# Performance work log

Measured on AMD Instinct MI355X. Metric: run time of the kernel, lower is better.

Reference implementation:

```python
import jax, jax.numpy as jnp
import numpy as np

N_NODES = 100000
N_EDGES = 640000
D = 128
N_LAYERS = 4
N_GRAPHS = 512


def setup_inputs() -> dict:
    key = jax.random.key(0)
    ks = jax.random.split(key, 12)
    x = jax.random.normal(ks[0], (N_NODES, D), dtype=jnp.float32)
    edge_index = jax.random.randint(ks[1], (2, N_EDGES), 0, N_NODES, dtype=jnp.int64)
    batch = jnp.sort(jax.random.randint(ks[2], (N_NODES,), 0, N_GRAPHS, dtype=jnp.int64))
    s = 1.0 / np.sqrt(D)
    convW = jax.random.uniform(ks[3], (N_LAYERS, D, D), jnp.float32, -s, s)
    convB = jax.random.uniform(ks[4], (N_LAYERS, D), jnp.float32, -s, s)
    W1 = jax.random.uniform(ks[5], (D, D), jnp.float32, -s, s)
    b1 = jax.random.uniform(ks[6], (D,), jnp.float32, -s, s)
    W2 = jax.random.uniform(ks[7], (D, D), jnp.float32, -s, s)
    b2 = jax.random.uniform(ks[8], (D,), jnp.float32, -s, s)
    W3 = jax.random.uniform(ks[9], (D, 1), jnp.float32, -s, s)
    b3 = jax.random.uniform(ks[10], (1,), jnp.float32, -s, s)
    return {"x": x, "edge_index": edge_index, "batch": batch,
            "convW": convW, "convB": convB,
            "W1": W1, "b1": b1, "W2": W2, "b2": b2, "W3": W3, "b3": b3}


def reference(x, edge_index, batch, convW, convB, W1, b1, W2, b2, W3, b3):
    N = x.shape[0]
    # GCNConv default: add self-loops, symmetric deg^-1/2 normalization
    loops = jnp.arange(N, dtype=edge_index.dtype)
    src = jnp.concatenate([edge_index[0], loops])  # [E+N]
    dst = jnp.concatenate([edge_index[1], loops])
    deg = jax.ops.segment_sum(jnp.ones_like(dst, dtype=x.dtype), dst, num_segments=N)
    dinv = jnp.where(deg > 0, jax.lax.rsqrt(deg), 0.0)
    norm = (dinv[src] * dinv[dst])[:, None]  # [E+N, 1]
    h = x
    for i in range(N_LAYERS):
        hw = h @ convW[i]                                   # [N, D]
        msg = hw[src] * norm                                # gather + scale [E+N, D]
        agg = jax.ops.segment_sum(msg, dst, num_segments=N)  # scatter-add [N, D]
        h = jax.nn.relu(agg + convB[i])
    pooled = jax.ops.segment_sum(h, batch, num_segments=N_GRAPHS)  # [G, D]
    z = jax.nn.relu(pooled @ W1 + b1)
    z = jax.nn.relu(z @ W2 + b2)
    return jax.nn.sigmoid(z @ W3 + b3)  # [G, 1]
```

## Files before the change

### kernel.cpp

```cpp
#include <hip/hip_runtime.h>
#include <math.h>

#define D 128
#define LSTRIDE 136
#define NPB 64

typedef _Float16 half8 __attribute__((ext_vector_type(8)));
typedef _Float16 half4v __attribute__((ext_vector_type(4)));
typedef _Float16 half2v __attribute__((ext_vector_type(2)));
typedef float f32x4 __attribute__((ext_vector_type(4)));


__global__ void k_count(const int* __restrict__ ei, int* __restrict__ counts,
                        int* __restrict__ pidx, int E) {
    int e0 = (blockIdx.x * blockDim.x + threadIdx.x) * 4;
    if (e0 + 3 < E) {
        int4 d4 = *(const int4*)(ei + E + e0);
        int4 p;
        p.x = atomicAdd(&counts[d4.x], 1);
        p.y = atomicAdd(&counts[d4.y], 1);
        p.z = atomicAdd(&counts[d4.z], 1);
        p.w = atomicAdd(&counts[d4.w], 1);
        *(int4*)(pidx + e0) = p;
    } else {
        for (int e = e0; e < E; e++) pidx[e] = atomicAdd(&counts[ei[E + e]], 1);
    }
}

__global__ __launch_bounds__(256) void k_scan1(const int* __restrict__ counts,
                                               int* __restrict__ rowptr,
                                               int* __restrict__ bsums,
                                               float* __restrict__ dinv, int N) {
    __shared__ int sh[256];
    const int t = threadIdx.x;
    const int base = blockIdx.x * 1024 + t * 4;
    int c[4];
#pragma unroll
    for (int j = 0; j < 4; j++) c[j] = (base + j < N) ? counts[base + j] : 0;
#pragma unroll
    for (int j = 0; j < 4; j++)
        if (base + j < N) dinv[base + j] = rsqrtf((float)(c[j] + 1));
    int tsum = c[0] + c[1] + c[2] + c[3];
    sh[t] = tsum;
    __syncthreads();
    for (int off = 1; off < 256; off <<= 1) {
        int v = (t >= off) ? sh[t - off] : 0;
        __syncthreads();
        sh[t] += v;
        __syncthreads();
    }
    int run = (t == 0) ? 0 : sh[t - 1];
    if (t == 255) bsums[blockIdx.x] = sh[255];
#pragma unroll
    for (int j = 0; j < 4; j++) {
        if (base + j <= N) rowptr[base + j] = run;
        run += c[j];
    }
}

__global__ __launch_bounds__(128) void k_scan2(int* __restrict__ bsums, int NB) {
    __shared__ int sh[128];
    const int t = threadIdx.x;
    sh[t] = (t < NB) ? bsums[t] : 0;
    __syncthreads();
    for (int off = 1; off < 128; off <<= 1) {
        int v = (t >= off) ? sh[t - off] : 0;
        __syncthreads();
        sh[t] += v;
        __syncthreads();
    }
    if (t < NB) bsums[t] = (t == 0) ? 0 : sh[t - 1];
}

__global__ void k_scan3(int* __restrict__ rowptr, const int* __restrict__ bsums, int N) {
    int i = blockIdx.x * blockDim.x + threadIdx.x;
    if (i <= N) rowptr[i] += bsums[i >> 10];
}

__global__ void k_fill(const int* __restrict__ ei, const int* __restrict__ rowptr,
                       const int* __restrict__ pidx, int* __restrict__ srcs, int E) {
    int e0 = (blockIdx.x * blockDim.x + threadIdx.x) * 4;
    if (e0 + 3 < E) {
        int4 s4 = *(const int4*)(ei + e0);
        int4 d4 = *(const int4*)(ei + E + e0);
        int4 p4 = *(const int4*)(pidx + e0);
        int r0 = rowptr[d4.x], r1 = rowptr[d4.y], r2 = rowptr[d4.z], r3 = rowptr[d4.w];
        srcs[r0 + p4.x] = s4.x;
        srcs[r1 + p4.y] = s4.y;
        srcs[r2 + p4.z] = s4.z;
        srcs[r3 + p4.w] = s4.w;
    } else {
        for (int e = e0; e < E; e++)
            srcs[rowptr[ei[E + e]] + pidx[e]] = ei[e];
    }
}


__global__ void k_cvt(const float* __restrict__ x, const float* __restrict__ dinv,
                      _Float16* __restrict__ y, int n8) {
    int i = blockIdx.x * blockDim.x + threadIdx.x;
    if (i >= n8) return;
    float s = dinv[i >> 4];
    const float4 v0 = *(const float4*)(x + (size_t)i * 8);
    const float4 v1 = *(const float4*)(x + (size_t)i * 8 + 4);
    half8 h;
    h[0] = (_Float16)(v0.x * s); h[1] = (_Float16)(v0.y * s);
    h[2] = (_Float16)(v0.z * s); h[3] = (_Float16)(v0.w * s);
    h[4] = (_Float16)(v1.x * s); h[5] = (_Float16)(v1.y * s);
    h[6] = (_Float16)(v1.z * s); h[7] = (_Float16)(v1.w * s);
    *(half8*)(y + (size_t)i * 8) = h;
}


__global__ __launch_bounds__(256) void k_prepw(const float* __restrict__ convW,
                                               _Float16* __restrict__ Wf) {
    const int l = blockIdx.x >> 3;
    const int slot = (blockIdx.x & 7) * 256 + threadIdx.x;
    const float* W = convW + (size_t)l * D * D;
    const int p = slot >> 6, ln = slot & 63;
    const int s = p >> 3, c = p & 7;
    const int kbase = s * 32 + ((ln >> 4) << 3);
    const int n = (c << 4) + (ln & 15);
    half8 hv;
#pragma unroll
    for (int j = 0; j < 8; j++) hv[j] = (_Float16)W[(size_t)(kbase + j) * D + n];
    *(half8*)(Wf + (size_t)l * D * D + (size_t)slot * 8) = hv;
}


__global__ __launch_bounds__(256) void k_layer(
        const _Float16* __restrict__ gin,
        const int* __restrict__ rowptr, const int* __restrict__ srcs,
        const float* __restrict__ dinv,
        const _Float16* __restrict__ Wf,
        const float* __restrict__ bias,
        _Float16* __restrict__ gout, int N, int last) {
    __shared__ _Float16 S[NPB * LSTRIDE];

    const int tid  = threadIdx.x;
    const int w    = tid >> 6;
    const int lane = tid & 63;
    const int q    = lane >> 4;
    const int l16  = lane & 15;
    const int nb0  = blockIdx.x * NPB;

    const int cb = l16 * 8;
    for (int it = 0; it < 4; ++it) {
        const int nl = w * 16 + q * 4 + it;
        const int node = nb0 + nl;
        float a[8];
#pragma unroll
        for (int j = 0; j < 8; j++) a[j] = 0.f;

        if (node < N) {
            half8 sv = *(const half8*)(gin + (size_t)node * D + cb);
#pragma unroll
            for (int j = 0; j < 8; j++) a[j] = (float)sv[j];
            const int beg = rowptr[node];
            const int end = rowptr[node + 1];
            int e = beg;
            for (; e + 3 < end; e += 4) {
                int s0 = srcs[e], s1 = srcs[e + 1], s2 = srcs[e + 2], s3 = srcs[e + 3];
                half8 v0 = *(const half8*)(gin + (size_t)s0 * D + cb);
                half8 v1 = *(const half8*)(gin + (size_t)s1 * D + cb);
                half8 v2 = *(const half8*)(gin + (size_t)s2 * D + cb);
                half8 v3 = *(const half8*)(gin + (size_t)s3 * D + cb);
#pragma unroll
                for (int j = 0; j < 8; j++)
                    a[j] += ((float)v0[j] + (float)v1[j]) + ((float)v2[j] + (float)v3[j]);
            }
            for (; e < end; e++) {
                int s0 = srcs[e];
                half8 v0 = *(const half8*)(gin + (size_t)s0 * D + cb);
#pragma unroll
                for (int j = 0; j < 8; j++) a[j] += (float)v0[j];
            }
        }
        const float sc = (node < N) ? dinv[node] : 0.f;
        half8 o;
#pragma unroll
        for (int j = 0; j < 8; j++) o[j] = (_Float16)(a[j] * sc);
        *(half8*)(&S[nl * LSTRIDE + cb]) = o;
    }
    __syncthreads();

    f32x4 acc[8];
#pragma unroll
    for (int cc = 0; cc < 8; cc++) acc[cc] = (f32x4){0.f, 0.f, 0.f, 0.f};

    const int nl = w * 16 + l16;
#pragma unroll
    for (int s = 0; s < 4; s++) {
        half8 bf = *(const half8*)(&S[nl * LSTRIDE + s * 32 + q * 8]);
#pragma unroll
        for (int cc = 0; cc < 8; cc++) {
            half8 wh = *(const half8*)(Wf + (size_t)((s * 8 + cc) * 64 + lane) * 8);
            acc[cc] = __builtin_amdgcn_mfma_f32_16x16x32_f16(wh, bf, acc[cc], 0, 0, 0);
        }
    }

    const int node = nb0 + nl;
    if (node < N) {
        const float scale = last ? 1.0f : dinv[node];
        _Float16* rp = gout + (size_t)node * D + q * 4;
#pragma unroll
        for (int cc = 0; cc < 8; cc++) {
            const float4 bc = *(const float4*)(bias + cc * 16 + q * 4);
            half4v o;
            o[0] = (_Float16)(fmaxf(acc[cc][0] + bc.x, 0.f) * scale);
            o[1] = (_Float16)(fmaxf(acc[cc][1] + bc.y, 0.f) * scale);
            o[2] = (_Float16)(fmaxf(acc[cc][2] + bc.z, 0.f) * scale);
            o[3] = (_Float16)(fmaxf(acc[cc][3] + bc.w, 0.f) * scale);
            *(half4v*)(rp + cc * 16) = o;
        }
    }
}


__global__ __launch_bounds__(256) void k_poolhead(
        const _Float16* __restrict__ h, const int* __restrict__ batch,
        const float* __restrict__ W1, const float* __restrict__ b1,
        const float* __restrict__ W2, const float* __restrict__ b2,
        const float* __restrict__ W3, const float* __restrict__ b3,
        float* __restrict__ out, int N) {
    __shared__ int sb[2];
    __shared__ float part[4][D];
    __shared__ float v[D];
    __shared__ float z[D];
    __shared__ float red[D];

    const int g = blockIdx.x;
    const int t = threadIdx.x;

    if (t < 2) {
        int target = g + t;
        int lo = 0, hi = N;
        while (lo < hi) {
            int mid = (lo + hi) >> 1;
            if (batch[mid] < target) lo = mid + 1; else hi = mid;
        }
        sb[t] = lo;
    }
    __syncthreads();
    const int rs = sb[0], re = sb[1];

    const int w = t >> 6;
    const int lane = t & 63;
    const int c = lane * 2;

    float ax = 0.f, ay = 0.f;
    for (int r = rs + w; r < re; r += 4) {
        half2v vv = *(const half2v*)(h + (size_t)r * D + c);
        ax += (float)vv[0]; ay += (float)vv[1];
    }
    part[w][c] = ax;
    part[w][c + 1] = ay;
    __syncthreads();

    if (t < D) v[t] = part[0][t] + part[1][t] + part[2][t] + part[3][t];
    __syncthreads();

    if (t < D) {
        float s = b1[t];
        for (int k = 0; k < D; k++) s = fmaf(v[k], W1[(size_t)k * D + t], s);
        z[t] = fmaxf(s, 0.f);
    }
    __syncthreads();

    if (t < D) {
        float s = b2[t];
        for (int k = 0; k < D; k++) s = fmaf(z[k], W2[(size_t)k * D + t], s);
        red[t] = fmaxf(s, 0.f) * W3[t];
    }
    __syncthreads();
    for (int off = 64; off >= 1; off >>= 1) {
        if (t < off) red[t] += red[t + off];
        __syncthreads();
    }
    if (t == 0) out[g] = 1.f / (1.f + expf(-(red[0] + b3[0])));
}


extern "C" void kernel_launch(void* const* d_in, const int* in_sizes, int n_in,
                              void* d_out, int out_size, void* d_ws, size_t ws_size,
                              hipStream_t stream) {
    const float* x     = (const float*)d_in[0];
    const int*   ei    = (const int*)d_in[1];
    const int*   batch = (const int*)d_in[2];
    const float* convW = (const float*)d_in[3];
    const float* convB = (const float*)d_in[4];
    const float* W1 = (const float*)d_in[5];
    const float* b1 = (const float*)d_in[6];
    const float* W2 = (const float*)d_in[7];
    const float* b2 = (const float*)d_in[8];
    const float* W3 = (const float*)d_in[9];
    const float* b3 = (const float*)d_in[10];
    float* out = (float*)d_out;

    const int N = in_sizes[0] / D;
    const int E = in_sizes[1] / 2;
    const int G = out_size;
    const int NB = (N + 1023) / 1024;

    char* w = (char*)d_ws;
    size_t off = 0;
    auto alloc = [&](size_t bytes) -> char* {
        char* p = w + off;
        off += (bytes + 255) & ~(size_t)255;
        return p;
    };
    float*     dinv   = (float*)alloc((size_t)N * 4);
    _Float16*  gA     = (_Float16*)alloc((size_t)N * D * 2);
    _Float16*  gB     = (_Float16*)alloc((size_t)N * D * 2);
    _Float16*  Wf     = (_Float16*)alloc((size_t)4 * D * D * 2);
    int*       counts = (int*)alloc((size_t)N * 4);
    int*       rowptr = (int*)alloc((size_t)(N + 1) * 4);
    int*       pidx   = (int*)alloc((size_t)E * 4);
    int*       srcs   = (int*)alloc((size_t)E * 4);
    int*       bsums  = (int*)alloc((size_t)NB * 4);

    hipMemsetAsync(counts, 0, (size_t)N * 4, stream);
    k_count<<<(E / 4 + 255) / 256, 256, 0, stream>>>(ei, counts, pidx, E);
    k_prepw<<<32, 256, 0, stream>>>(convW, Wf);
    k_scan1<<<NB, 256, 0, stream>>>(counts, rowptr, bsums, dinv, N);
    k_cvt<<<(N * D / 8 + 255) / 256, 256, 0, stream>>>(x, dinv, gA, N * D / 8);
    k_scan2<<<1, 128, 0, stream>>>(bsums, NB);
    k_scan3<<<(N + 1 + 255) / 256, 256, 0, stream>>>(rowptr, bsums, N);
    k_fill<<<(E / 4 + 255) / 256, 256, 0, stream>>>(ei, rowptr, pidx, srcs, E);

    const int layer_grid = (N + NPB - 1) / NPB;
    const _Float16* gi = gA;
    _Float16* go = gB;
    for (int l = 0; l < 4; l++) {
        k_layer<<<layer_grid, 256, 0, stream>>>(gi, rowptr, srcs, dinv,
                                                Wf + (size_t)l * D * D,
                                                convB + (size_t)l * D,
                                                go, N, l == 3);
        const _Float16* tmp = go;
        go = (_Float16*)gi;
        gi = tmp;
    }

    k_poolhead<<<G, 256, 0, stream>>>(gi, batch, W1, b1, W2, b2, W3, b3, out, N);
}
```

Baseline: 388.7 us.

## Gather straight into MFMA operand registers and fuse block-sum scan into fixup

The layer kernel now has each wave own 16 nodes and each lane gather the 32 feature columns of one node that it later feeds to MFMA as the B operand. This removes the LDS staging buffer and the block-wide barrier. Within a wave, nodes are processed in lockstep two edges per step until the longest neighbour list in the wave is done, so lanes with short lists sit idle. Each row is read by only four lanes, so memory access is less coalesced than before. Separately, the single-block scan of block sums is folded into the rowptr fixup kernel: each block redoes the small prefix scan, which saves one kernel launch.

```diff
diff --git a/kernel.cpp b/kernel.cpp
--- a/kernel.cpp
+++ b/kernel.cpp
@@ -2,8 +2,6 @@
 #include <math.h>
 
 #define D 128
-#define LSTRIDE 136
-#define NPB 64
 
 typedef _Float16 half8 __attribute__((ext_vector_type(8)));
 typedef _Float16 half4v __attribute__((ext_vector_type(4)));
@@ -58,23 +56,24 @@
     }
 }
 
-__global__ __launch_bounds__(128) void k_scan2(int* __restrict__ bsums, int NB) {
-    __shared__ int sh[128];
+__global__ __launch_bounds__(256) void k_scan3(int* __restrict__ rowptr,
+                                               const int* __restrict__ bsums,
+                                               int NB, int N) {
+    __shared__ int pre[128];
     const int t = threadIdx.x;
-    sh[t] = (t < NB) ? bsums[t] : 0;
+    if (t < 128) pre[t] = (t < NB) ? bsums[t] : 0;
     __syncthreads();
     for (int off = 1; off < 128; off <<= 1) {
-        int v = (t >= off) ? sh[t - off] : 0;
-        __syncthreads();
-        sh[t] += v;
-        __syncthreads();
-    }
-    if (t < NB) bsums[t] = (t == 0) ? 0 : sh[t - 1];
-}
-
-__global__ void k_scan3(int* __restrict__ rowptr, const int* __restrict__ bsums, int N) {
-    int i = blockIdx.x * blockDim.x + threadIdx.x;
-    if (i <= N) rowptr[i] += bsums[i >> 10];
+        int v = (t >= off && t < 128) ? pre[t - off] : 0;
+        __syncthreads();
+        if (t < 128) pre[t] += v;
+        __syncthreads();
+    }
+    int i = blockIdx.x * blockDim.x + t;
+    if (i <= N) {
+        int b = i >> 10;
+        rowptr[i] += (b == 0) ? 0 : pre[b - 1];
+    }
 }
 
 __global__ void k_fill(const int* __restrict__ ei, const int* __restrict__ rowptr,
@@ -135,71 +134,85 @@
         const _Float16* __restrict__ Wf,
         const float* __restrict__ bias,
         _Float16* __restrict__ gout, int N, int last) {
-    __shared__ _Float16 S[NPB * LSTRIDE];
-
-    const int tid  = threadIdx.x;
-    const int w    = tid >> 6;
-    const int lane = tid & 63;
+    const int gtid = blockIdx.x * 256 + threadIdx.x;
+    const int wid  = gtid >> 6;
+    const int lane = threadIdx.x & 63;
     const int q    = lane >> 4;
     const int l16  = lane & 15;
-    const int nb0  = blockIdx.x * NPB;
-
-    const int cb = l16 * 8;
-    for (int it = 0; it < 4; ++it) {
-        const int nl = w * 16 + q * 4 + it;
-        const int node = nb0 + nl;
-        float a[8];
-#pragma unroll
-        for (int j = 0; j < 8; j++) a[j] = 0.f;
-
-        if (node < N) {
-            half8 sv = *(const half8*)(gin + (size_t)node * D + cb);
-#pragma unroll
-            for (int j = 0; j < 8; j++) a[j] = (float)sv[j];
-            const int beg = rowptr[node];
-            const int end = rowptr[node + 1];
-            int e = beg;
-            for (; e + 3 < end; e += 4) {
-                int s0 = srcs[e], s1 = srcs[e + 1], s2 = srcs[e + 2], s3 = srcs[e + 3];
-                half8 v0 = *(const half8*)(gin + (size_t)s0 * D + cb);
-                half8 v1 = *(const half8*)(gin + (size_t)s1 * D + cb);
-                half8 v2 = *(const half8*)(gin + (size_t)s2 * D + cb);
-                half8 v3 = *(const half8*)(gin + (size_t)s3 * D + cb);
-#pragma unroll
-                for (int j = 0; j < 8; j++)
-                    a[j] += ((float)v0[j] + (float)v1[j]) + ((float)v2[j] + (float)v3[j]);
+    const int node = wid * 16 + l16;
+    const int nodec = (node < N) ? node : (N - 1);
+
+    float af[4][8];
+    {
+        const _Float16* grow = gin + (size_t)nodec * D + q * 8;
+#pragma unroll
+        for (int s = 0; s < 4; s++) {
+            half8 v = *(const half8*)(grow + s * 32);
+#pragma unroll
+            for (int j = 0; j < 8; j++) af[s][j] = (float)v[j];
+        }
+    }
+
+    int e = rowptr[nodec];
+    const int end = rowptr[nodec + 1];
+    while (__any(e < end)) {
+        const int rem = end - e;
+        if (rem >= 2) {
+            int s0 = srcs[e], s1 = srcs[e + 1];
+            const _Float16* r0 = gin + (size_t)s0 * D + q * 8;
+            const _Float16* r1 = gin + (size_t)s1 * D + q * 8;
+            half8 a0 = *(const half8*)(r0);
+            half8 a1 = *(const half8*)(r0 + 32);
+            half8 a2 = *(const half8*)(r0 + 64);
+            half8 a3 = *(const half8*)(r0 + 96);
+            half8 b0 = *(const half8*)(r1);
+            half8 b1 = *(const half8*)(r1 + 32);
+            half8 b2 = *(const half8*)(r1 + 64);
+            half8 b3 = *(const half8*)(r1 + 96);
+#pragma unroll
+            for (int j = 0; j < 8; j++) {
+                af[0][j] += (float)a0[j] + (float)b0[j];
+                af[1][j] += (float)a1[j] + (float)b1[j];
+                af[2][j] += (float)a2[j] + (float)b2[j];
+                af[3][j] += (float)a3[j] + (float)b3[j];
             }
-            for (; e < end; e++) {
-                int s0 = srcs[e];
-                half8 v0 = *(const half8*)(gin + (size_t)s0 * D + cb);
-#pragma unroll
-                for (int j = 0; j < 8; j++) a[j] += (float)v0[j];
+        } else if (rem == 1) {
+            int s0 = srcs[e];
+            const _Float16* r0 = gin + (size_t)s0 * D + q * 8;
+            half8 a0 = *(const half8*)(r0);
+            half8 a1 = *(const half8*)(r0 + 32);
+            half8 a2 = *(const half8*)(r0 + 64);
+            half8 a3 = *(const half8*)(r0 + 96);
+#pragma unroll
+            for (int j = 0; j < 8; j++) {
+                af[0][j] += (float)a0[j];
+                af[1][j] += (float)a1[j];
+                af[2][j] += (float)a2[j];
+                af[3][j] += (float)a3[j];
             }
         }
-        const float sc = (node < N) ? dinv[node] : 0.f;
-        half8 o;
-#pragma unroll
-        for (int j = 0; j < 8; j++) o[j] = (_Float16)(a[j] * sc);
-        *(half8*)(&S[nl * LSTRIDE + cb]) = o;
-    }
-    __syncthreads();
+        e += 2;
+    }
+
+    const float sc = dinv[nodec];
+    half8 bf[4];
+#pragma unroll
+    for (int s = 0; s < 4; s++)
+#pragma unroll
+        for (int j = 0; j < 8; j++) bf[s][j] = (_Float16)(af[s][j] * sc);
 
     f32x4 acc[8];
 #pragma unroll
     for (int cc = 0; cc < 8; cc++) acc[cc] = (f32x4){0.f, 0.f, 0.f, 0.f};
-
-    const int nl = w * 16 + l16;
 #pragma unroll
     for (int s = 0; s < 4; s++) {
-        half8 bf = *(const half8*)(&S[nl * LSTRIDE + s * 32 + q * 8]);
 #pragma unroll
         for (int cc = 0; cc < 8; cc++) {
             half8 wh = *(const half8*)(Wf + (size_t)((s * 8 + cc) * 64 + lane) * 8);
-            acc[cc] = __builtin_amdgcn_mfma_f32_16x16x32_f16(wh, bf, acc[cc], 0, 0, 0);
-        }
-    }
-
-    const int node = nb0 + nl;
+            acc[cc] = __builtin_amdgcn_mfma_f32_16x16x32_f16(wh, bf[s], acc[cc], 0, 0, 0);
+        }
+    }
+
     if (node < N) {
         const float scale = last ? 1.0f : dinv[node];
         _Float16* rp = gout + (size_t)node * D + q * 4;
@@ -324,11 +337,11 @@
     k_prepw<<<32, 256, 0, stream>>>(convW, Wf);
     k_scan1<<<NB, 256, 0, stream>>>(counts, rowptr, bsums, dinv, N);
     k_cvt<<<(N * D / 8 + 255) / 256, 256, 0, stream>>>(x, dinv, gA, N * D / 8);
-    k_scan2<<<1, 128, 0, stream>>>(bsums, NB);
-    k_scan3<<<(N + 1 + 255) / 256, 256, 0, stream>>>(rowptr, bsums, N);
+    k_scan3<<<(N + 1 + 255) / 256, 256, 0, stream>>>(rowptr, bsums, NB, N);
     k_fill<<<(E / 4 + 255) / 256, 256, 0, stream>>>(ei, rowptr, pidx, srcs, E);
 
-    const int layer_grid = (N + NPB - 1) / NPB;
+    const int nwaves = (N + 15) / 16;
+    const int layer_grid = (nwaves * 64 + 255) / 256;
     const _Float16* gi = gA;
     _Float16* go = gB;
     for (int l = 0; l < 4; l++) {
```

Result: no change. 393.8 us (+1.3%).

## Merge scan kernels and double layer block to 128 nodes with 512 threads

Applied to the files above, without the earlier changes.

Folds the block-sum scan into the rowptr fixup kernel, so every block redundantly scans the small bsums array in shared memory and one launch is removed. Also enlarges the GCN layer tile from 64 to 128 nodes per block with 512 threads, which amortises the weight-tile loads over more nodes. The bigger shared buffer and thread count may lower occupancy, and the hidden parts of the layer kernel must index correctly with 8 waves.

```diff
diff --git a/kernel.cpp b/kernel.cpp
--- a/kernel.cpp
+++ b/kernel.cpp
@@ -3,7 +3,6 @@
 
 #define D 128
 #define LSTRIDE 136
-#define NPB 64
 
 typedef _Float16 half8 __attribute__((ext_vector_type(8)));
 typedef _Float16 half4v __attribute__((ext_vector_type(4)));
@@ -58,23 +57,24 @@
     }
 }
 
-__global__ __launch_bounds__(128) void k_scan2(int* __restrict__ bsums, int NB) {
-    __shared__ int sh[128];
+__global__ __launch_bounds__(256) void k_scan3(int* __restrict__ rowptr,
+                                               const int* __restrict__ bsums,
+                                               int NB, int N) {
+    __shared__ int pre[128];
     const int t = threadIdx.x;
-    sh[t] = (t < NB) ? bsums[t] : 0;
+    if (t < 128) pre[t] = (t < NB) ? bsums[t] : 0;
     __syncthreads();
     for (int off = 1; off < 128; off <<= 1) {
-        int v = (t >= off) ? sh[t - off] : 0;
-        __syncthreads();
-        sh[t] += v;
-        __syncthreads();
-    }
-    if (t < NB) bsums[t] = (t == 0) ? 0 : sh[t - 1];
-}
-
-__global__ void k_scan3(int* __restrict__ rowptr, const int* __restrict__ bsums, int N) {
-    int i = blockIdx.x * blockDim.x + threadIdx.x;
-    if (i <= N) rowptr[i] += bsums[i >> 10];
+        int v = (t >= off && t < 128) ? pre[t - off] : 0;
+        __syncthreads();
+        if (t < 128) pre[t] += v;
+        __syncthreads();
+    }
+    int i = blockIdx.x * blockDim.x + t;
+    if (i <= N) {
+        int b = i >> 10;
+        rowptr[i] += (b == 0) ? 0 : pre[b - 1];
+    }
 }
 
 __global__ void k_fill(const int* __restrict__ ei, const int* __restrict__ rowptr,
@@ -128,21 +128,21 @@
 }
 
 
-__global__ __launch_bounds__(256) void k_layer(
+__global__ __launch_bounds__(512) void k_layer(
         const _Float16* __restrict__ gin,
         const int* __restrict__ rowptr, const int* __restrict__ srcs,
         const float* __restrict__ dinv,
         const _Float16* __restrict__ Wf,
         const float* __restrict__ bias,
         _Float16* __restrict__ gout, int N, int last) {
-    __shared__ _Float16 S[NPB * LSTRIDE];
+    __shared__ _Float16 S[128 * LSTRIDE];
 
     const int tid  = threadIdx.x;
     const int w    = tid >> 6;
     const int lane = tid & 63;
     const int q    = lane >> 4;
     const int l16  = lane & 15;
-    const int nb0  = blockIdx.x * NPB;
+    const int nb0  = blockIdx.x * 128;
 
     const int cb = l16 * 8;
     for (int it = 0; it < 4; ++it) {
@@ -324,15 +324,14 @@
     k_prepw<<<32, 256, 0, stream>>>(convW, Wf);
     k_scan1<<<NB, 256, 0, stream>>>(counts, rowptr, bsums, dinv, N);
     k_cvt<<<(N * D / 8 + 255) / 256, 256, 0, stream>>>(x, dinv, gA, N * D / 8);
-    k_scan2<<<1, 128, 0, stream>>>(bsums, NB);
-    k_scan3<<<(N + 1 + 255) / 256, 256, 0, stream>>>(rowptr, bsums, N);
+    k_scan3<<<(N + 1 + 255) / 256, 256, 0, stream>>>(rowptr, bsums, NB, N);
     k_fill<<<(E / 4 + 255) / 256, 256, 0, stream>>>(ei, rowptr, pidx, srcs, E);
 
-    const int layer_grid = (N + NPB - 1) / NPB;
+    const int layer_grid = (N + 127) / 128;
     const _Float16* gi = gA;
     _Float16* go = gB;
     for (int l = 0; l < 4; l++) {
-        k_layer<<<layer_grid, 256, 0, stream>>>(gi, rowptr, srcs, dinv,
+        k_layer<<<layer_grid, 512, 0, stream>>>(gi, rowptr, srcs, dinv,
                                                 Wf + (size_t)l * D * D,
                                                 convB + (size_t)l * D,
                                                 go, N, l == 3);
```

Measured after the change: 360.5 us. -7.2%, faster.
